# Kernel optimization log

Measured on AMD Instinct MI355X. Metric: run time of the kernel, lower is better.

Reference implementation:

```python
import jax, jax.numpy as jnp
import numpy as np

ARITY = 3
GROUPS = 1024
OUT_DIM = 8
BATCH = 4096
ACT_FACTOR = 1.0


def setup_inputs() -> dict:
    key = jax.random.key(0)
    k1, k2 = jax.random.split(key)
    X = jax.random.normal(k1, (BATCH, GROUPS * ARITY), dtype=jnp.float32)
    params = jax.random.normal(k2, (GROUPS, 3 ** ARITY, OUT_DIM), dtype=jnp.float32)
    return {"X": X, "params": params}


def reference(X, params):
    G, T, D = params.shape          # groups, 3**arity, out_dim
    B = X.shape[0]
    r = X.shape[1] // G             # arity
    A = X.reshape(B, G, r)
    ref_ind = (3 ** r - 1) // 2     # sum(3**i for i in range(r))

    A_abs = jnp.abs(A)
    A_ind = jnp.argsort(A_abs, axis=2)                       # [B,G,r]
    A_sort = jnp.take_along_axis(A_abs, A_ind, axis=2)       # sorted |A|
    sgn = jnp.where(A >= 0, 1, -1)
    A_sgn = jnp.take_along_axis(sgn, A_ind, axis=2)          # signs in sorted order

    # piecewise-linear coefficients: smallest magnitude then successive gaps
    coef = jnp.concatenate([A_sort[:, :, :1], A_sort[:, :, 1:] - A_sort[:, :, :-1]], axis=2)

    # reverse cumulative sum of signed base-3 digits -> table indices
    terms = A_sgn * jnp.power(3, A_ind)                      # int32 [B,G,r]
    idx = jnp.flip(jnp.cumsum(jnp.flip(terms, axis=2), axis=2), axis=2) + ref_ind

    # gather per (batch, group, rank): params[g, idx[b,g,k], :]
    gathered = params[jnp.arange(G)[None, :, None], idx]     # [B,G,r,D]
    out = jnp.einsum('bgrd,bgr->bgd', gathered, coef)        # [B,G,D]
    return out.reshape(B, G * D) * ACT_FACTOR
```

## Files before the change

kernel.cpp:

```cpp
#include <hip/hip_runtime.h>


#define B_BATCH 4096
#define N_GROUPS 1024
#define N_TERMS 27
#define OUT_DIM 8
#define GC 16
#define BC 128
#define ROW_STRIDE 220

typedef float floatx4 __attribute__((ext_vector_type(4)));

__global__ __launch_bounds__(256)
void hoa_kernel(const float* __restrict__ X,
                const float* __restrict__ P,
                float* __restrict__ out) {
    __shared__ float lds[GC * ROW_STRIDE];

    const int tid = threadIdx.x;
    const int g0 = blockIdx.x * GC;
    const int b0 = blockIdx.y * BC;

    {
        const floatx4* P4 = (const floatx4*)(P + (size_t)g0 * (N_TERMS * OUT_DIM));
        floatx4* L4 = (floatx4*)lds;
        for (int i = tid; i < GC * 54; i += 256) {
            const int r = i / 54;
            const int c = i - r * 54;
            L4[r * (ROW_STRIDE / 4) + c] = P4[i];
        }
    }
    __syncthreads();

    const int g_local = tid & (GC - 1);
    const int b_slot = tid >> 4;
    const float* lg = lds + g_local * ROW_STRIDE;
    const int g = g0 + g_local;

    #pragma unroll 4
    for (int it = 0; it < BC / 16; ++it) {
        const int b = b0 + b_slot + it * 16;

        const float* xp = X + (size_t)b * (N_GROUPS * 3) + g * 3;
        const float A0 = xp[0];
        const float A1 = xp[1];
        const float A2 = xp[2];

        float m0 = fabsf(A0), m1 = fabsf(A1), m2 = fabsf(A2);
        int t0 = (A0 >= 0.0f) ? 1 : -1;
        int t1 = (A1 >= 0.0f) ? 3 : -3;
        int t2 = (A2 >= 0.0f) ? 9 : -9;

        if (m0 > m1) { float tm=m0; m0=m1; m1=tm; int tt=t0; t0=t1; t1=tt; }
        if (m1 > m2) { float tm=m1; m1=m2; m2=tm; int tt=t1; t1=t2; t2=tt; }
        if (m0 > m1) { float tm=m0; m0=m1; m1=tm; int tt=t0; t0=t1; t1=tt; }

        const float c0 = m0;
        const float c1 = m1 - m0;
        const float c2 = m2 - m1;

        const int i2 = 13 + t2;
        const int i1 = i2 + t1;
        const int i0 = i1 + t0;

        const floatx4* r0 = (const floatx4*)(lg + i0 * OUT_DIM);
        const floatx4* r1 = (const floatx4*)(lg + i1 * OUT_DIM);
        const floatx4* r2 = (const floatx4*)(lg + i2 * OUT_DIM);
        const floatx4 g0a = r0[0], g0b = r0[1];
        const floatx4 g1a = r1[0], g1b = r1[1];
        const floatx4 g2a = r2[0], g2b = r2[1];

        const floatx4 oa = c0 * g0a + c1 * g1a + c2 * g2a;
        const floatx4 ob = c0 * g0b + c1 * g1b + c2 * g2b;

        floatx4* op = (floatx4*)(out + (size_t)b * (N_GROUPS * OUT_DIM) + g * OUT_DIM);
        op[0] = oa;
        op[1] = ob;
    }
}

extern "C" void kernel_launch(void* const* d_in, const int* in_sizes, int n_in,
                              void* d_out, int out_size, void* d_ws, size_t ws_size,
                              hipStream_t stream) {
    const float* X = (const float*)d_in[0];
    const float* P = (const float*)d_in[1];
    float* out = (float*)d_out;

    dim3 grid(N_GROUPS / GC, B_BATCH / BC);
    hoa_kernel<<<grid, 256, 0, stream>>>(X, P, out);
}
```

Baseline: 36.63 us.

## Store parameter table in LDS as bf16 and double batch chunk per block

Converts the per-group parameter rows to packed bf16 with round-to-nearest-even when staging into shared memory, halving LDS footprint and reducing each gathered row to a single 16-byte LDS read. It also doubles the batch rows per block so the table staging cost is amortized over more work. This trades numerical precision of the parameters (bf16 instead of fp32) for fewer LDS transactions, and it adds unpack ALU work plus scalar global loads during staging.

```diff
diff --git a/kernel.cpp b/kernel.cpp
--- a/kernel.cpp
+++ b/kernel.cpp
@@ -6,35 +6,42 @@
 #define N_TERMS 27
 #define OUT_DIM 8
 #define GC 16
-#define BC 128
-#define ROW_STRIDE 220
+#define BC 256
+#define ROWD 116
+#define NPAIR 108
 
 typedef float floatx4 __attribute__((ext_vector_type(4)));
+
+__device__ __forceinline__ unsigned int bf16_rne_lo(unsigned int u) {
+    return (u + 0x7fffu + ((u >> 16) & 1u)) >> 16;
+}
+__device__ __forceinline__ unsigned int bf16_rne_hi(unsigned int u) {
+    return (u + 0x7fffu + ((u >> 16) & 1u)) & 0xffff0000u;
+}
 
 __global__ __launch_bounds__(256)
 void hoa_kernel(const float* __restrict__ X,
                 const float* __restrict__ P,
                 float* __restrict__ out) {
-    __shared__ float lds[GC * ROW_STRIDE];
+    __shared__ unsigned int ldsb[GC * ROWD];
 
     const int tid = threadIdx.x;
     const int g0 = blockIdx.x * GC;
     const int b0 = blockIdx.y * BC;
 
-    {
-        const floatx4* P4 = (const floatx4*)(P + (size_t)g0 * (N_TERMS * OUT_DIM));
-        floatx4* L4 = (floatx4*)lds;
-        for (int i = tid; i < GC * 54; i += 256) {
-            const int r = i / 54;
-            const int c = i - r * 54;
-            L4[r * (ROW_STRIDE / 4) + c] = P4[i];
-        }
+    for (int i = tid; i < GC * NPAIR; i += 256) {
+        const int r = i / NPAIR;
+        const int c = i - r * NPAIR;
+        const float* src = P + (size_t)(g0 + r) * (N_TERMS * OUT_DIM) + 2 * c;
+        const unsigned int lo = bf16_rne_lo(__float_as_uint(src[0]));
+        const unsigned int hi = bf16_rne_hi(__float_as_uint(src[1]));
+        ldsb[r * ROWD + c] = lo | hi;
     }
     __syncthreads();
 
     const int g_local = tid & (GC - 1);
-    const int b_slot = tid >> 4;
-    const float* lg = lds + g_local * ROW_STRIDE;
+    const int b_slot  = tid >> 4;
+    const unsigned int* lg = ldsb + g_local * ROWD;
     const int g = g0 + g_local;
 
     #pragma unroll 4
@@ -63,15 +70,35 @@
         const int i1 = i2 + t1;
         const int i0 = i1 + t0;
 
-        const floatx4* r0 = (const floatx4*)(lg + i0 * OUT_DIM);
-        const floatx4* r1 = (const floatx4*)(lg + i1 * OUT_DIM);
-        const floatx4* r2 = (const floatx4*)(lg + i2 * OUT_DIM);
-        const floatx4 g0a = r0[0], g0b = r0[1];
-        const floatx4 g1a = r1[0], g1b = r1[1];
-        const floatx4 g2a = r2[0], g2b = r2[1];
+        const uint4 q0 = *(const uint4*)(lg + i0 * 4);
+        const uint4 q1 = *(const uint4*)(lg + i1 * 4);
+        const uint4 q2 = *(const uint4*)(lg + i2 * 4);
 
-        const floatx4 oa = c0 * g0a + c1 * g1a + c2 * g2a;
-        const floatx4 ob = c0 * g0b + c1 * g1b + c2 * g2b;
+        floatx4 oa, ob;
+        oa.x = c0 * __uint_as_float(q0.x << 16)
+             + c1 * __uint_as_float(q1.x << 16)
+             + c2 * __uint_as_float(q2.x << 16);
+        oa.y = c0 * __uint_as_float(q0.x & 0xffff0000u)
+             + c1 * __uint_as_float(q1.x & 0xffff0000u)
+             + c2 * __uint_as_float(q2.x & 0xffff0000u);
+        oa.z = c0 * __uint_as_float(q0.y << 16)
+             + c1 * __uint_as_float(q1.y << 16)
+             + c2 * __uint_as_float(q2.y << 16);
+        oa.w = c0 * __uint_as_float(q0.y & 0xffff0000u)
+             + c1 * __uint_as_float(q1.y & 0xffff0000u)
+             + c2 * __uint_as_float(q2.y & 0xffff0000u);
+        ob.x = c0 * __uint_as_float(q0.z << 16)
+             + c1 * __uint_as_float(q1.z << 16)
+             + c2 * __uint_as_float(q2.z << 16);
+        ob.y = c0 * __uint_as_float(q0.z & 0xffff0000u)
+             + c1 * __uint_as_float(q1.z & 0xffff0000u)
+             + c2 * __uint_as_float(q2.z & 0xffff0000u);
+        ob.z = c0 * __uint_as_float(q0.w << 16)
+             + c1 * __uint_as_float(q1.w << 16)
+             + c2 * __uint_as_float(q2.w << 16);
+        ob.w = c0 * __uint_as_float(q0.w & 0xffff0000u)
+             + c1 * __uint_as_float(q1.w & 0xffff0000u)
+             + c2 * __uint_as_float(q2.w & 0xffff0000u);
 
         floatx4* op = (floatx4*)(out + (size_t)b * (N_GROUPS * OUT_DIM) + g * OUT_DIM);
         op[0] = oa;
```

Result: slower. 38.28 us (+4.5%).
